# Kernel optimization log

Measured on AMD Instinct MI355X. Metric: run time of the kernel, lower is better.

## Reference

```python
import jax, jax.numpy as jnp
import numpy as np

B, S, D, H = 32, 577, 768, 12
DH = D // H
MLP = 4 * D
EPS = 1e-5


def _layernorm(x, g, b):
    m = jnp.mean(x, axis=-1, keepdims=True)
    v = jnp.mean((x - m) ** 2, axis=-1, keepdims=True)
    return (x - m) * jax.lax.rsqrt(v + EPS) * g + b


def setup_inputs() -> dict:
    key = jax.random.key(0)
    ks = jax.random.split(key, 12)
    w = lambda k, shp: (jax.random.normal(k, shp, dtype=jnp.float32) * 0.02)
    return {
        "x": jax.random.normal(ks[0], (B, S, D), dtype=jnp.float32),
        "ln1_g": jnp.ones((D,), jnp.float32), "ln1_b": jnp.zeros((D,), jnp.float32),
        "ln2_g": jnp.ones((D,), jnp.float32), "ln2_b": jnp.zeros((D,), jnp.float32),
        "wq": w(ks[1], (H, DH, DH)), "bq": jnp.zeros((H, DH), jnp.float32),
        "wk": w(ks[2], (H, DH, DH)), "bk": jnp.zeros((H, DH), jnp.float32),
        "wv": w(ks[3], (H, DH, DH)), "bv": jnp.zeros((H, DH), jnp.float32),
        "w1": w(ks[4], (D, MLP)), "b1": jnp.zeros((MLP,), jnp.float32),
        "w2": w(ks[5], (MLP, D)), "b2": jnp.zeros((D,), jnp.float32),
    }


def reference(x, ln1_g, ln1_b, ln2_g, ln2_b, wq, bq, wk, bk, wv, bv, w1, b1, w2, b2):
    b, s, d = x.shape
    xn = _layernorm(x, ln1_g, ln1_b)
    xh = xn.reshape(b, s, H, DH)  # split heads along last dim (as in torch slicing)
    # per-head linear maps, batched over heads: [B,H,S,DH]
    q = jnp.einsum('bshd,hdo->bhso', xh, wq) + bq[:, None, :]
    k = jnp.einsum('bshd,hdo->bhso', xh, wk) + bk[:, None, :]
    v = jnp.einsum('bshd,hdo->bhso', xh, wv) + bv[:, None, :]
    scores = jnp.einsum('bhso,bhto->bhst', q, k) / (DH ** 0.5)
    attn = jax.nn.softmax(scores, axis=-1)  # softmax over keys (torch dim=1 of [S,S])
    o = jnp.einsum('bhst,bhtd->bshd', attn, v).reshape(b, s, d)
    out = x + o
    yn = _layernorm(out, ln2_g, ln2_b)
    h = jax.nn.gelu(yn @ w1 + b1, approximate=False)  # torch GELU default is erf-based
    return out + h @ w2 + b2
```

## Files before the change

### kernel.cpp

```cpp
#include <hip/hip_runtime.h>

#define S_LEN 577
#define SPAD  640
#define DMODEL 768
#define NH 12
#define DHEAD 64
#define MLPD 3072
#define NROWS (32 * 577)
#define MPAD  18688
#define NBH   (32 * 12)
#define LOG2E 1.44269504088896340736f

typedef __attribute__((ext_vector_type(8))) short s8v;
typedef __attribute__((ext_vector_type(4))) float f4v;

#define MFMA16(a, b, c) __builtin_amdgcn_mfma_f32_16x16x32_bf16((a), (b), (c), 0, 0, 0)

__device__ __forceinline__ short f2bf(float f) {
  union { float f; unsigned u; } a; a.f = f;
  unsigned r = a.u + 0x7FFFu + ((a.u >> 16) & 1u);
  return (short)(r >> 16);
}
__device__ __forceinline__ short f2bfF(float f) {
  union { float f; unsigned u; } a; a.f = f;
  return (short)((a.u + 0x8000u) >> 16);
}

__device__ __forceinline__ void gload16(const short* g, const short* l) {
  __builtin_amdgcn_global_load_lds(
      (const __attribute__((address_space(1))) void*)g,
      (__attribute__((address_space(3))) void*)l, 16, 0, 0);
}

__global__ __launch_bounds__(256) void transpose_w(const float* __restrict__ in,
                                                   short* __restrict__ out, int R, int C) {
  __shared__ float tile[32][33];
  int c0 = blockIdx.x * 32, r0 = blockIdx.y * 32;
  int tx = threadIdx.x, ty = threadIdx.y;
  for (int i = ty; i < 32; i += 8) tile[i][tx] = in[(size_t)(r0 + i) * C + c0 + tx];
  __syncthreads();
  for (int i = ty; i < 32; i += 8) out[(size_t)(c0 + i) * R + r0 + tx] = f2bf(tile[tx][i]);
}

__global__ __launch_bounds__(256) void prep_qkv(const float* __restrict__ wq, const float* __restrict__ wk,
                                                const float* __restrict__ wv, short* __restrict__ oq,
                                                short* __restrict__ ok, short* __restrict__ ov) {
  int h = blockIdx.x, t = threadIdx.x;
  const float* src0 = wq + (size_t)h * 4096;
  const float* src1 = wk + (size_t)h * 4096;
  const float* src2 = wv + (size_t)h * 4096;
  short* dst0 = oq + (size_t)h * 4096;
  short* dst1 = ok + (size_t)h * 4096;
  short* dst2 = ov + (size_t)h * 4096;
  for (int i = t; i < 4096; i += 256) {
    int o = i >> 6, d = i & 63;
    dst0[i] = f2bf(src0[d * 64 + o]);
    dst1[i] = f2bf(src1[d * 64 + o]);
    dst2[i] = f2bf(src2[d * 64 + o]);
  }
}

__global__ __launch_bounds__(256) void pad_kv(short* __restrict__ kg, short* __restrict__ vt) {
  int idx = blockIdx.x * 256 + threadIdx.x;
  const int padw = SPAD - S_LEN;
  const int per = DHEAD * padw;
  if (idx >= NBH * per) return;
  int bh = idx / per, r = idx - bh * per;
  int col = r / padw, s = S_LEN + (r - col * padw);
  vt[((size_t)bh * DHEAD + col) * SPAD + s] = 0;
  kg[((size_t)bh * SPAD + s) * DHEAD + col] = 0;
}

__global__ __launch_bounds__(256) void ln_kernel(const float* __restrict__ x, const float* __restrict__ g,
                                                 const float* __restrict__ bta, short* __restrict__ out) {
  int row = blockIdx.x;
  int t = threadIdx.x;
  const float* xr = x + (size_t)row * DMODEL;
  float v0 = xr[t], v1 = xr[t + 256], v2 = xr[t + 512];
  float s = v0 + v1 + v2;
  float s2 = v0 * v0 + v1 * v1 + v2 * v2;
  for (int o = 32; o; o >>= 1) { s += __shfl_down(s, o); s2 += __shfl_down(s2, o); }
  __shared__ float red[8];
  if ((t & 63) == 0) { int w = t >> 6; red[w] = s; red[4 + w] = s2; }
  __syncthreads();
  s = red[0] + red[1] + red[2] + red[3];
  s2 = red[4] + red[5] + red[6] + red[7];
  float m = s * (1.f / DMODEL);
  float rs = rsqrtf(s2 * (1.f / DMODEL) - m * m + 1e-5f);
  short* orow = out + (size_t)row * DMODEL;
  orow[t]       = f2bf((v0 - m) * rs * g[t]       + bta[t]);
  orow[t + 256] = f2bf((v1 - m) * rs * g[t + 256] + bta[t + 256]);
  orow[t + 512] = f2bf((v2 - m) * rs * g[t + 512] + bta[t + 512]);
}

__global__ __launch_bounds__(256) void qkv_kernel(const short* __restrict__ xn,
    const short* __restrict__ wqt, const short* __restrict__ wkt, const short* __restrict__ wvt,
    const float* __restrict__ bq, const float* __restrict__ bk, const float* __restrict__ bv,
    short* __restrict__ qg, short* __restrict__ kg, short* __restrict__ vt) {
  __shared__ __align__(16) short wl[3][64][72];
  int bid = blockIdx.x;
  int h = bid % NH, mt = bid / NH;
  int t = threadIdx.x;
  {
    int o = t >> 2, d0 = (t & 3) * 16;
    const short* s0 = wqt + (size_t)h * 4096 + o * 64 + d0;
    const short* s1 = wkt + (size_t)h * 4096 + o * 64 + d0;
    const short* s2 = wvt + (size_t)h * 4096 + o * 64 + d0;
    *(uint4*)&wl[0][o][d0]     = *(const uint4*)s0;
    *(uint4*)&wl[0][o][d0 + 8] = *(const uint4*)(s0 + 8);
    *(uint4*)&wl[1][o][d0]     = *(const uint4*)s1;
    *(uint4*)&wl[1][o][d0 + 8] = *(const uint4*)(s1 + 8);
    *(uint4*)&wl[2][o][d0]     = *(const uint4*)s2;
    *(uint4*)&wl[2][o][d0 + 8] = *(const uint4*)(s2 + 8);
  }
  __syncthreads();
  int w = t >> 6, l = t & 63, l15 = l & 15, lh = l >> 4;
  int m0 = mt * 64 + w * 16;
  if (m0 >= NROWS) return;
  f4v z = {0.f, 0.f, 0.f, 0.f};
  f4v aq[4], ak[4], av[4];
#pragma unroll
  for (int nt = 0; nt < 4; ++nt) { aq[nt] = z; ak[nt] = z; av[nt] = z; }
  const short* xrow = xn + (size_t)(m0 + l15) * DMODEL + h * DHEAD;
#pragma unroll
  for (int kk = 0; kk < 64; kk += 32) {
    s8v af = *(const s8v*)(xrow + kk + lh * 8);
#pragma unroll
    for (int nt = 0; nt < 4; ++nt) {
      s8v b0 = *(const s8v*)&wl[0][nt * 16 + l15][kk + lh * 8];
      s8v b1 = *(const s8v*)&wl[1][nt * 16 + l15][kk + lh * 8];
      s8v b2 = *(const s8v*)&wl[2][nt * 16 + l15][kk + lh * 8];
      aq[nt] = MFMA16(af, b0, aq[nt]);
      ak[nt] = MFMA16(af, b1, ak[nt]);
      av[nt] = MFMA16(af, b2, av[nt]);
    }
  }
#pragma unroll
  for (int nt = 0; nt < 4; ++nt) {
    int col = nt * 16 + l15;
    float biq = bq[h * DHEAD + col], bik = bk[h * DHEAD + col], biv = bv[h * DHEAD + col];
#pragma unroll
    for (int i = 0; i < 4; ++i) {
      int m = m0 + lh * 4 + i;
      int bb = m / S_LEN;
      int ss = m - bb * S_LEN;
      int bh = bb * NH + h;
      qg[((size_t)bh * S_LEN + ss) * DHEAD + col] = f2bf((aq[nt][i] + biq) * (0.125f * LOG2E));
      kg[((size_t)bh * SPAD + ss) * DHEAD + col]  = f2bf(ak[nt][i] + bik);
      vt[((size_t)bh * DHEAD + col) * SPAD + ss]  = f2bf(av[nt][i] + biv);
    }
  }
}

__global__ __launch_bounds__(64) void attn_kernel(const short* __restrict__ qg, const short* __restrict__ kg,
                                                  const short* __restrict__ vt, const float* __restrict__ x,
                                                  float* __restrict__ outp) {
  __shared__ __align__(16) short Pb[2][32][72];
  int bh = blockIdx.x;
  int qt = blockIdx.y;
  int h = bh % NH, b = bh / NH;
  int l = threadIdx.x & 63, l15 = l & 15, lh = l >> 4;
  int q0 = qt * 32;
  size_t qbase = (size_t)bh * S_LEN * DHEAD;
  size_t kbase = (size_t)bh * SPAD * DHEAD;
  size_t vbase = (size_t)bh * DHEAD * SPAD;
  s8v aq[2][2];
#pragma unroll
  for (int f = 0; f < 2; ++f) {
    int qrow = q0 + f * 16 + l15; if (qrow > 576) qrow = 576;
    const short* qp = qg + qbase + (size_t)qrow * DHEAD + lh * 8;
    aq[f][0] = *(const s8v*)qp;
    aq[f][1] = *(const s8v*)(qp + 32);
  }
  f4v z = {0.f, 0.f, 0.f, 0.f};
  f4v z16 = {-16.f, -16.f, -16.f, -16.f};
  f4v acc[2][4];
  float lsum[2][4];
#pragma unroll
  for (int f = 0; f < 2; ++f) {
#pragma unroll
    for (int dt = 0; dt < 4; ++dt) acc[f][dt] = z;
#pragma unroll
    for (int i = 0; i < 4; ++i) lsum[f][i] = 0.f;
  }

  s8v kf0[4], kf1[4], vf[2][4];
  f4v sc[2][4];

#define LOADK(KB)                                                      \
  {                                                                    \
    _Pragma("unroll")                                                  \
    for (int nt = 0; nt < 4; ++nt) {                                   \
      const short* kp = kg + kbase + (size_t)((KB) + nt * 16 + l15) * DHEAD + lh * 8; \
      kf0[nt] = *(const s8v*)kp;                                       \
      kf1[nt] = *(const s8v*)(kp + 32);                                \
    }                                                                  \
  }

#define LOADV(KB)                                                      \
  {                                                                    \
    _Pragma("unroll")                                                  \
    for (int kk2 = 0; kk2 < 2; ++kk2) {                                \
      const short* vp = vt + vbase + (KB) + kk2 * 32 + lh * 8;         \
      _Pragma("unroll")                                                \
      for (int dt = 0; dt < 4; ++dt)                                   \
        vf[kk2][dt] = *(const s8v*)(vp + (size_t)(dt * 16 + l15) * SPAD); \
    }                                                                  \
  }

#define QKT()                                                          \
  {                                                                    \
    __builtin_amdgcn_s_setprio(1);                                     \
    _Pragma("unroll")                                                  \
    for (int nt = 0; nt < 4; ++nt) {                                   \
      _Pragma("unroll")                                                \
      for (int f = 0; f < 2; ++f) {                                    \
        f4v a = MFMA16(aq[f][0], kf0[nt], z16);                        \
        a = MFMA16(aq[f][1], kf1[nt], a);                              \
        sc[f][nt] = a;                                                 \
      }                                                                \
    }                                                                  \
    __builtin_amdgcn_s_setprio(0);                                     \
  }

#define MASK9()                                                        \
  {                                                                    \
    _Pragma("unroll")                                                  \
    for (int nt = 0; nt < 4; ++nt) {                                   \
      int col = 576 + nt * 16 + l15;                                   \
      if (col > 576) {                                                 \
        _Pragma("unroll")                                              \
        for (int f = 0; f < 2; ++f) {                                  \
          sc[f][nt][0] = sc[f][nt][1] = sc[f][nt][2] = sc[f][nt][3] = -1e30f; } \
      }                                                                \
    }                                                                  \
  }

#define SMAX(PAR)                                                      \
  {                                                                    \
    _Pragma("unroll")                                                  \
    for (int f = 0; f < 2; ++f)                                        \
      _Pragma("unroll")                                                \
      for (int i = 0; i < 4; ++i) {                                    \
        float s = lsum[f][i];                                          \
        _Pragma("unroll")                                              \
        for (int nt = 0; nt < 4; ++nt) {                               \
          float e = exp2f(sc[f][nt][i]);                               \
          s += e;                                                      \
          Pb[PAR][f * 16 + lh * 4 + i][nt * 16 + l15] = f2bfF(e);      \
        }                                                              \
        lsum[f][i] = s;                                                \
      }                                                                \
  }

#define PVT(PAR)                                                       \
  {                                                                    \
    __builtin_amdgcn_s_setprio(1);                                     \
    _Pragma("unroll")                                                  \
    for (int kk2 = 0; kk2 < 2; ++kk2) {                                \
      s8v af0 = *(const s8v*)&Pb[PAR][l15][kk2 * 32 + lh * 8];         \
      s8v af1 = *(const s8v*)&Pb[PAR][16 + l15][kk2 * 32 + lh * 8];    \
      _Pragma("unroll")                                                \
      for (int dt = 0; dt < 4; ++dt) {                                 \
        acc[0][dt] = MFMA16(af0, vf[kk2][dt], acc[0][dt]);             \
        acc[1][dt] = MFMA16(af1, vf[kk2][dt], acc[1][dt]);             \
      }                                                                \
    }                                                                  \
    __builtin_amdgcn_s_setprio(0);                                     \
  }

  LOADK(0);
  QKT();
  LOADK(64);
  SMAX(0);

  for (int kt = 0; kt < 10; ++kt) {
    int par = kt & 1;
    LOADV(kt * 64);
    if (kt < 9) {
      QKT();
      if (kt < 8) LOADK((kt + 2) * 64);
      if (kt == 8) MASK9();
      SMAX(par ^ 1);
    }
    PVT(par);
  }
#undef LOADK
#undef LOADV
#undef QKT
#undef MASK9
#undef SMAX
#undef PVT
#pragma unroll
  for (int f = 0; f < 2; ++f)
#pragma unroll
    for (int i = 0; i < 4; ++i) {
      float s = lsum[f][i];
      s += __shfl_xor(s, 1);
      s += __shfl_xor(s, 2);
      s += __shfl_xor(s, 4);
      s += __shfl_xor(s, 8);
      int srow = q0 + f * 16 + lh * 4 + i;
      if (srow > 576) continue;
      float inv = __builtin_amdgcn_rcpf(s);
      size_t idx0 = ((size_t)b * S_LEN + srow) * DMODEL + h * DHEAD + l15;
#pragma unroll
      for (int dt = 0; dt < 4; ++dt) {
        size_t idx = idx0 + dt * 16;
        outp[idx] = x[idx] + acc[f][dt][i] * inv;
      }
    }
}

#define BARR asm volatile("s_barrier" ::: "memory")

#define STAGE_HALF(G, SH, bufi, half, ktile)                                       \
  do {                                                                             \
    _Pragma("unroll") for (int rd = 0; rd < 2; ++rd) {                             \
      int rw_ = rd * 64 + (tid >> 3);                                              \
      int sl_ = (tid & 7) ^ (rw_ & 7);                                             \
      gload16((G) + (size_t)((half) * 128 + rw_) * K + (ktile) * 64 + sl_ * 8,     \
              &SH[bufi][(half) * 128 + rw_][(tid & 7) * 8]);                       \
    }                                                                              \
  } while (0)

#define READ_A(rh)                                                                 \
  _Pragma("unroll") for (int mt = 0; mt < 4; ++mt)                                 \
    _Pragma("unroll") for (int kh = 0; kh < 2; ++kh)                               \
      af[mt][kh] = *(const s8v*)&sA[cur][(rh) * 128 + wr * 64 + mt * 16 + l15]     \
                                    [((kh * 4 + lh) ^ s7) * 8];

#define READ_B(BF, chh)                                                            \
  _Pragma("unroll") for (int nt = 0; nt < 2; ++nt)                                 \
    _Pragma("unroll") for (int kh = 0; kh < 2; ++kh)                               \
      BF[nt][kh] = *(const s8v*)&sB[cur][wc * 64 + (chh) * 32 + nt * 16 + l15]     \
                                    [((kh * 4 + lh) ^ s7) * 8];

#define DO_MFMA(rh, ch, BF)                                                        \
  __builtin_amdgcn_s_setprio(1);                                                   \
  _Pragma("unroll") for (int mt = 0; mt < 4; ++mt)                                 \
    _Pragma("unroll") for (int nt = 0; nt < 2; ++nt)                               \
      _Pragma("unroll") for (int kh = 0; kh < 2; ++kh)                             \
        acc[(rh) * 4 + mt][(ch) * 2 + nt] =                                        \
            MFMA16(af[mt][kh], BF[nt][kh], acc[(rh) * 4 + mt][(ch) * 2 + nt]);     \
  __builtin_amdgcn_s_setprio(0);

#define GEMM8_BODY                                                                 \
  int nwg = gridDim.x;                                                             \
  int orig = blockIdx.x;                                                           \
  int qq = nwg >> 3, rr = nwg & 7;                                                 \
  int xcd = orig & 7, lin = orig >> 3;                                             \
  int wg = (xcd < rr ? xcd * (qq + 1) : rr * (qq + 1) + (xcd - rr) * qq) + lin;    \
  int nx = N >> 8;                                                                 \
  int n0 = (wg % nx) * 256, m0 = (wg / nx) * 256;                                  \
  int tid = threadIdx.x;                                                           \
  int wid = tid >> 6, l = tid & 63, l15 = l & 15, lh = l >> 4;                     \
  int s7 = l15 & 7;                                                                \
  int wr = wid >> 2, wc = wid & 3;                                                 \
  const short* Ab = A + (size_t)m0 * K;                                            \
  const short* Bb = Bt + (size_t)n0 * K;                                           \
  f4v z = {0.f, 0.f, 0.f, 0.f};                                                    \
  f4v acc[8][4];                                                                   \
  _Pragma("unroll") for (int i = 0; i < 8; ++i)                                    \
    _Pragma("unroll") for (int j = 0; j < 4; ++j) acc[i][j] = z;                   \
  s8v af[4][2], bf0[2][2], bf1[2][2];                                              \
  int NT = K >> 6;                                                                 \
  STAGE_HALF(Ab, sA, 0, 0, 0); STAGE_HALF(Ab, sA, 0, 1, 0);                        \
  STAGE_HALF(Bb, sB, 0, 0, 0); STAGE_HALF(Bb, sB, 0, 1, 0);                        \
  STAGE_HALF(Ab, sA, 1, 0, 1); STAGE_HALF(Bb, sB, 1, 0, 1);                        \
  STAGE_HALF(Bb, sB, 1, 1, 1);                                                     \
  asm volatile("s_waitcnt vmcnt(6)" ::: "memory");                                 \
  BARR;                                                                            \
  int cur = 0;                                                                     \
  for (int kt = 0; kt < NT; ++kt) {                                                \
    int nxt = cur ^ 1;                                                             \
    READ_A(0); READ_B(bf0, 0);                                                     \
    if (kt + 1 < NT) STAGE_HALF(Ab, sA, nxt, 1, kt + 1);                           \
    BARR; DO_MFMA(0, 0, bf0); BARR;                                                \
    READ_B(bf1, 1);                                                                \
    if (kt + 2 < NT) STAGE_HALF(Ab, sA, cur, 0, kt + 2);                           \
    BARR; DO_MFMA(0, 1, bf1); BARR;                                                \
    READ_A(1);                                                                     \
    if (kt + 2 < NT) STAGE_HALF(Bb, sB, cur, 0, kt + 2);                           \
    BARR; DO_MFMA(1, 1, bf1); BARR;                                                \
    if (kt + 2 < NT) STAGE_HALF(Bb, sB, cur, 1, kt + 2);                           \
    BARR; DO_MFMA(1, 0, bf0);                                                      \
    if (kt < NT - 2)       { asm volatile("s_waitcnt vmcnt(6)" ::: "memory"); }    \
    else if (kt == NT - 2) { asm volatile("s_waitcnt vmcnt(0)" ::: "memory"); }    \
    BARR;                                                                          \
    cur = nxt;                                                                     \
  }

__global__ __launch_bounds__(512, 1) void gemm_gelu(const short* __restrict__ A, const short* __restrict__ Bt,
                                                    const float* __restrict__ bias, short* __restrict__ C,
                                                    int M, int N, int K) {
  __shared__ __align__(16) short sA[2][256][64];
  __shared__ __align__(16) short sB[2][256][64];
  GEMM8_BODY
#pragma unroll
  for (int ri = 0; ri < 8; ++ri)
#pragma unroll
    for (int ci = 0; ci < 4; ++ci) {
      int col = n0 + wc * 64 + (ci >> 1) * 32 + (ci & 1) * 16 + l15;
      float bi = bias[col];
#pragma unroll
      for (int i = 0; i < 4; ++i) {
        int row = m0 + (ri >> 2) * 128 + wr * 64 + (ri & 3) * 16 + lh * 4 + i;
        float v = acc[ri][ci][i] + bi;
        float u = v * (2.30221838f + 0.10294364f * v * v);
        v = v * __builtin_amdgcn_rcpf(1.f + exp2f(-u));
        C[(size_t)row * N + col] = f2bfF(v);
      }
    }
}

__global__ __launch_bounds__(512, 1) void gemm_res(const short* __restrict__ A, const short* __restrict__ Bt,
                                                   const float* __restrict__ bias, float* __restrict__ outp,
                                                   int Mvalid, int N, int K) {
  __shared__ __align__(16) short sA[2][256][64];
  __shared__ __align__(16) short sB[2][256][64];
  GEMM8_BODY
#pragma unroll
  for (int ri = 0; ri < 8; ++ri)
#pragma unroll
    for (int ci = 0; ci < 4; ++ci) {
      int col = n0 + wc * 64 + (ci >> 1) * 32 + (ci & 1) * 16 + l15;
      float bi = bias[col];
#pragma unroll
      for (int i = 0; i < 4; ++i) {
        int row = m0 + (ri >> 2) * 128 + wr * 64 + (ri & 3) * 16 + lh * 4 + i;
        if (row < Mvalid) {
          size_t idx = (size_t)row * N + col;
          outp[idx] += acc[ri][ci][i] + bi;
        }
      }
    }
}

extern "C" void kernel_launch(void* const* d_in, const int* in_sizes, int n_in,
                              void* d_out, int out_size, void* d_ws, size_t ws_size,
                              hipStream_t stream) {
  const float* x    = (const float*)d_in[0];
  const float* ln1g = (const float*)d_in[1];
  const float* ln1b = (const float*)d_in[2];
  const float* ln2g = (const float*)d_in[3];
  const float* ln2b = (const float*)d_in[4];
  const float* wq   = (const float*)d_in[5];
  const float* bq   = (const float*)d_in[6];
  const float* wk   = (const float*)d_in[7];
  const float* bk   = (const float*)d_in[8];
  const float* wv   = (const float*)d_in[9];
  const float* bv   = (const float*)d_in[10];
  const float* w1   = (const float*)d_in[11];
  const float* b1   = (const float*)d_in[12];
  const float* w2   = (const float*)d_in[13];
  const float* b2   = (const float*)d_in[14];
  float* outp = (float*)d_out;

  char* ws = (char*)d_ws;
  size_t off = 0;
  auto carve = [&](size_t elems) -> short* {
    short* p = (short*)(ws + off);
    off += elems * sizeof(short);
    off = (off + 255) & ~(size_t)255;
    return p;
  };
  short* yn   = carve((size_t)MPAD * DMODEL);
  short* w1t  = carve((size_t)MLPD * DMODEL);
  short* w2t  = carve((size_t)DMODEL * MLPD);
  short* wqt  = carve((size_t)NH * 64 * 64);
  short* wkt  = carve((size_t)NH * 64 * 64);
  short* wvt  = carve((size_t)NH * 64 * 64);
  size_t union_base = off;
  short* hbuf = carve((size_t)MPAD * MLPD);
  off = union_base;
  short* xn   = carve((size_t)NROWS * DMODEL);
  short* qg   = carve((size_t)NBH * S_LEN * DHEAD);
  short* kg   = carve((size_t)NBH * SPAD * DHEAD);
  short* vtb  = carve((size_t)NBH * DHEAD * SPAD);
  (void)ws_size; (void)in_sizes; (void)n_in; (void)out_size;

  transpose_w<<<dim3(MLPD / 32, DMODEL / 32), dim3(32, 8), 0, stream>>>(w1, w1t, DMODEL, MLPD);
  transpose_w<<<dim3(DMODEL / 32, MLPD / 32), dim3(32, 8), 0, stream>>>(w2, w2t, MLPD, DMODEL);
  prep_qkv<<<NH, 256, 0, stream>>>(wq, wk, wv, wqt, wkt, wvt);
  pad_kv<<<(NBH * DHEAD * (SPAD - S_LEN) + 255) / 256, 256, 0, stream>>>(kg, vtb);

  ln_kernel<<<NROWS, 256, 0, stream>>>(x, ln1g, ln1b, xn);

  qkv_kernel<<<((NROWS + 63) / 64) * NH, 256, 0, stream>>>(xn, wqt, wkt, wvt, bq, bk, bv, qg, kg, vtb);

  attn_kernel<<<dim3(NBH, 19), 64, 0, stream>>>(qg, kg, vtb, x, outp);

  ln_kernel<<<NROWS, 256, 0, stream>>>(outp, ln2g, ln2b, yn);

  gemm_gelu<<<dim3((MPAD / 256) * (MLPD / 256)), 512, 0, stream>>>(yn, w1t, b1, hbuf, MPAD, MLPD, DMODEL);
  gemm_res<<<dim3((MPAD / 256) * (DMODEL / 256)), 512, 0, stream>>>(hbuf, w2t, b2, outp, NROWS, DMODEL, MLPD);
}
```

Measured before the change: 497.2 us.

## Process 64 query rows per attention block to double K/V reuse

Each single-wave attention block now handles 64 query rows (four 16-row fragments) instead of 32, which halves the grid to 10 query tiles. Every K and V fragment loaded from global memory is reused across twice as many rows, and the QK^T/softmax work is split into two halves to keep score registers bounded. The cost is more accumulator registers per wave and fewer blocks for the GPU to schedule, which may reduce latency hiding, plus a larger LDS buffer.

```diff
diff --git a/kernel.cpp b/kernel.cpp
--- a/kernel.cpp
+++ b/kernel.cpp
@@ -152,21 +152,21 @@
   }
 }
 
-__global__ __launch_bounds__(64) void attn_kernel(const short* __restrict__ qg, const short* __restrict__ kg,
-                                                  const short* __restrict__ vt, const float* __restrict__ x,
-                                                  float* __restrict__ outp) {
-  __shared__ __align__(16) short Pb[2][32][72];
+__global__ __launch_bounds__(64, 2) void attn_kernel(const short* __restrict__ qg, const short* __restrict__ kg,
+                                                     const short* __restrict__ vt, const float* __restrict__ x,
+                                                     float* __restrict__ outp) {
+  __shared__ __align__(16) short Pb[2][64][72];
   int bh = blockIdx.x;
   int qt = blockIdx.y;
   int h = bh % NH, b = bh / NH;
   int l = threadIdx.x & 63, l15 = l & 15, lh = l >> 4;
-  int q0 = qt * 32;
+  int q0 = qt * 64;
   size_t qbase = (size_t)bh * S_LEN * DHEAD;
   size_t kbase = (size_t)bh * SPAD * DHEAD;
   size_t vbase = (size_t)bh * DHEAD * SPAD;
-  s8v aq[2][2];
-#pragma unroll
-  for (int f = 0; f < 2; ++f) {
+  s8v aq[4][2];
+#pragma unroll
+  for (int f = 0; f < 4; ++f) {
     int qrow = q0 + f * 16 + l15; if (qrow > 576) qrow = 576;
     const short* qp = qg + qbase + (size_t)qrow * DHEAD + lh * 8;
     aq[f][0] = *(const s8v*)qp;
@@ -174,10 +174,10 @@
   }
   f4v z = {0.f, 0.f, 0.f, 0.f};
   f4v z16 = {-16.f, -16.f, -16.f, -16.f};
-  f4v acc[2][4];
-  float lsum[2][4];
-#pragma unroll
-  for (int f = 0; f < 2; ++f) {
+  f4v acc[4][4];
+  float lsum[4][4];
+#pragma unroll
+  for (int f = 0; f < 4; ++f) {
 #pragma unroll
     for (int dt = 0; dt < 4; ++dt) acc[f][dt] = z;
 #pragma unroll
@@ -208,48 +208,46 @@
     }                                                                  \
   }
 
-#define QKT()                                                          \
+#define QKT_H(FH)                                                      \
   {                                                                    \
     __builtin_amdgcn_s_setprio(1);                                     \
     _Pragma("unroll")                                                  \
     for (int nt = 0; nt < 4; ++nt) {                                   \
       _Pragma("unroll")                                                \
-      for (int f = 0; f < 2; ++f) {                                    \
-        f4v a = MFMA16(aq[f][0], kf0[nt], z16);                        \
-        a = MFMA16(aq[f][1], kf1[nt], a);                              \
-        sc[f][nt] = a;                                                 \
+      for (int fo = 0; fo < 2; ++fo) {                                 \
+        f4v a = MFMA16(aq[2 * (FH) + fo][0], kf0[nt], z16);            \
+        a = MFMA16(aq[2 * (FH) + fo][1], kf1[nt], a);                  \
+        sc[fo][nt] = a;                                                \
       }                                                                \
     }                                                                  \
     __builtin_amdgcn_s_setprio(0);                                     \
   }
 
-#define MASK9()                                                        \
+#define SMAX_H(FH, PAR, MASK)                                          \
   {                                                                    \
-    _Pragma("unroll")                                                  \
-    for (int nt = 0; nt < 4; ++nt) {                                   \
-      int col = 576 + nt * 16 + l15;                                   \
-      if (col > 576) {                                                 \
-        _Pragma("unroll")                                              \
-        for (int f = 0; f < 2; ++f) {                                  \
-          sc[f][nt][0] = sc[f][nt][1] = sc[f][nt][2] = sc[f][nt][3] = -1e30f; } \
+    if (MASK) {                                                        \
+      _Pragma("unroll")                                                \
+      for (int nt = 0; nt < 4; ++nt) {                                 \
+        int col = 576 + nt * 16 + l15;                                 \
+        if (col > 576) {                                               \
+          _Pragma("unroll")                                            \
+          for (int fo = 0; fo < 2; ++fo) {                             \
+            sc[fo][nt][0] = sc[fo][nt][1] = sc[fo][nt][2] = sc[fo][nt][3] = -1e30f; } \
+        }                                                              \
       }                                                                \
     }                                                                  \
-  }
-
-#define SMAX(PAR)                                                      \
-  {                                                                    \
     _Pragma("unroll")                                                  \
-    for (int f = 0; f < 2; ++f)                                        \
+    for (int fo = 0; fo < 2; ++fo)                                     \
       _Pragma("unroll")                                                \
       for (int i = 0; i < 4; ++i) {                                    \
-        float s = lsum[f][i];                                          \
+        float s = lsum[2 * (FH) + fo][i];                              \
         _Pragma("unroll")                                              \
         for (int nt = 0; nt < 4; ++nt) {                               \
-          float e = exp2f(sc[f][nt][i]);                               \
+          float e = exp2f(sc[fo][nt][i]);                              \
           s += e;                                                      \
-          Pb[PAR][f * 16 + lh * 4 + i][nt * 16 + l15] = f2bfF(e);      \
+          Pb[PAR][(2 * (FH) + fo) * 16 + lh * 4 + i][nt * 16 + l15] = f2bfF(e); \
         }                                                              \
-        lsum[f][i] = s;                                                \
+        lsum[2 * (FH) + fo][i] = s;                                    \
       }                                                                \
   }
 
@@ -258,41 +256,44 @@
     __builtin_amdgcn_s_setprio(1);                                     \
     _Pragma("unroll")                                                  \
     for (int kk2 = 0; kk2 < 2; ++kk2) {                                \
-      s8v af0 = *(const s8v*)&Pb[PAR][l15][kk2 * 32 + lh * 8];         \
-      s8v af1 = *(const s8v*)&Pb[PAR][16 + l15][kk2 * 32 + lh * 8];    \
       _Pragma("unroll")                                                \
-      for (int dt = 0; dt < 4; ++dt) {                                 \
-        acc[0][dt] = MFMA16(af0, vf[kk2][dt], acc[0][dt]);             \
-        acc[1][dt] = MFMA16(af1, vf[kk2][dt], acc[1][dt]);             \
+      for (int f = 0; f < 4; ++f) {                                    \
+        s8v af = *(const s8v*)&Pb[PAR][f * 16 + l15][kk2 * 32 + lh * 8]; \
+        _Pragma("unroll")                                              \
+        for (int dt = 0; dt < 4; ++dt)                                 \
+          acc[f][dt] = MFMA16(af, vf[kk2][dt], acc[f][dt]);            \
       }                                                                \
     }                                                                  \
     __builtin_amdgcn_s_setprio(0);                                     \
   }
 
   LOADK(0);
-  QKT();
+  QKT_H(0);
+  SMAX_H(0, 0, false);
+  QKT_H(1);
   LOADK(64);
-  SMAX(0);
+  SMAX_H(1, 0, false);
 
   for (int kt = 0; kt < 10; ++kt) {
     int par = kt & 1;
     LOADV(kt * 64);
     if (kt < 9) {
-      QKT();
+      bool mask = (kt == 8);
+      QKT_H(0);
+      SMAX_H(0, par ^ 1, mask);
+      QKT_H(1);
       if (kt < 8) LOADK((kt + 2) * 64);
-      if (kt == 8) MASK9();
-      SMAX(par ^ 1);
+      SMAX_H(1, par ^ 1, mask);
     }
     PVT(par);
   }
 #undef LOADK
 #undef LOADV
-#undef QKT
-#undef MASK9
-#undef SMAX
+#undef QKT_H
+#undef SMAX_H
 #undef PVT
 #pragma unroll
-  for (int f = 0; f < 2; ++f)
+  for (int f = 0; f < 4; ++f)
 #pragma unroll
     for (int i = 0; i < 4; ++i) {
       float s = lsum[f][i];
@@ -489,7 +490,7 @@
 
   qkv_kernel<<<((NROWS + 63) / 64) * NH, 256, 0, stream>>>(xn, wqt, wkt, wvt, bq, bk, bv, qg, kg, vtb);
 
-  attn_kernel<<<dim3(NBH, 19), 64, 0, stream>>>(qg, kg, vtb, x, outp);
+  attn_kernel<<<dim3(NBH, 10), 64, 0, stream>>>(qg, kg, vtb, x, outp);
 
   ln_kernel<<<NROWS, 256, 0, stream>>>(outp, ln2g, ln2b, yn);
 
```

After: 452.5 us. 9.0% less time.
